# Performance work log

Hardware: AMD Instinct MI355X
Metric: run time of the kernel (lower is better)

## Reference

```python
import jax, jax.numpy as jnp
import numpy as np

B, S, E, H = 2, 2048, 1024, 16
DH = E // H


def setup_inputs() -> dict:
    key = jax.random.key(0)
    ks = jax.random.split(key, 9)
    s = 1.0 / np.sqrt(E)
    return {
        "queries": jax.random.normal(ks[0], (B, S, E), dtype=jnp.float32),
        "keys": jax.random.normal(ks[1], (B, S, E), dtype=jnp.float32),
        "values": jax.random.normal(ks[2], (B, S, E), dtype=jnp.float32),
        "mask": jax.random.randint(ks[3], (B, 1, 1, S), 0, 2, dtype=jnp.int32),
        "Wq": jax.random.normal(ks[4], (E, E), dtype=jnp.float32) * s,
        "Wk": jax.random.normal(ks[5], (E, E), dtype=jnp.float32) * s,
        "Wv": jax.random.normal(ks[6], (E, E), dtype=jnp.float32) * s,
        "Wo": jax.random.normal(ks[7], (E, E), dtype=jnp.float32) * s,
        "bo": jax.random.normal(ks[8], (E,), dtype=jnp.float32) * s,
    }


def reference(queries, keys, values, mask, Wq, Wk, Wv, Wo, bo):
    n, d_q, _ = queries.shape
    d_k = keys.shape[1]
    # Linear projections (torch Linear: x @ W.T), then split into heads
    q = (queries @ Wq.T).reshape(n, d_q, H, DH)
    k = (keys @ Wk.T).reshape(n, d_k, H, DH)
    v = (values @ Wv.T).reshape(n, d_k, H, DH)
    # [n, H, d_q, d_k] attention scores
    energy = jnp.einsum("nqhd,nkhd->nhqk", q, k)
    energy = jnp.where(mask == 0, jnp.float32(-1e20), energy)
    # NOTE: original scales by sqrt(key seq length), not head dim -- kept faithful
    attn = jax.nn.softmax(energy / jnp.sqrt(jnp.float32(d_k)), axis=3)
    out = jnp.einsum("nhql,nlhd->nqhd", attn, v).reshape(n, d_q, E)
    return out @ Wo.T + bo
```

## Files before the change

### kernel.cpp

```cpp
#include <hip/hip_runtime.h>
#include <hip/hip_bf16.h>

#define BB 2
#define SS 2048
#define EE 1024
#define HH 16
#define DHH 64

using bf16x8 = __attribute__((ext_vector_type(8))) __bf16;
using f32x4  = __attribute__((ext_vector_type(4))) float;

#if __has_builtin(__builtin_amdgcn_exp2f)
#define EXP2(x) __builtin_amdgcn_exp2f(x)
#else
#define EXP2(x) __exp2f(x)
#endif

static __device__ __forceinline__ unsigned short f2bf(float f) {
    unsigned int u = __float_as_uint(f);
    u += 0x7FFFu + ((u >> 16) & 1u);
    return (unsigned short)(u >> 16);
}

static __device__ __forceinline__ unsigned int pk2bf(float lo, float hi) {
    union { __hip_bfloat162 h2; unsigned int u; } c;
    c.h2 = __float22bfloat162_rn(float2{lo, hi});
    return c.u;
}

static __device__ __forceinline__ void async_load16(const void* g, void* l) {
    __builtin_amdgcn_global_load_lds(
        (const __attribute__((address_space(1))) unsigned int*)g,
        (__attribute__((address_space(3))) unsigned int*)l, 16, 0, 0);
}

__global__ void cvt_kernel(const float* __restrict__ W0, const float* __restrict__ W1,
                           const float* __restrict__ W2, const float* __restrict__ W3,
                           const float* __restrict__ X0, const float* __restrict__ X1,
                           const float* __restrict__ X2,
                           unsigned short* __restrict__ Wb,
                           unsigned short* __restrict__ D0, unsigned short* __restrict__ D1,
                           unsigned short* __restrict__ D2)
{
    const int z = blockIdx.y;
    const float* src;
    unsigned short* dst;
    if (z < 4) {
        if (blockIdx.x >= 512) return;
        src = (z == 0) ? W0 : (z == 1) ? W1 : (z == 2) ? W2 : W3;
        dst = Wb + (size_t)z * 1048576;
    } else {
        src = (z == 4) ? X0 : (z == 5) ? X1 : X2;
        dst = (z == 4) ? D0 : (z == 5) ? D1 : D2;
    }
    const size_t base = (size_t)blockIdx.x * 2048 + (size_t)threadIdx.x * 8;
    const float4 f0 = *(const float4*)(src + base);
    const float4 f1 = *(const float4*)(src + base + 4);
    uint4 p;
    p.x = pk2bf(f0.x, f0.y); p.y = pk2bf(f0.z, f0.w);
    p.z = pk2bf(f1.x, f1.y); p.w = pk2bf(f1.z, f1.w);
    *(uint4*)(dst + base) = p;
}

template<int MT, int NT, bool BF16OUT, bool VT_Z2>
__global__ __launch_bounds__(256, 3)
void gemm_xwt(const unsigned short* __restrict__ X0, const unsigned short* __restrict__ X1,
              const unsigned short* __restrict__ X2,
              const unsigned short* __restrict__ W0, const unsigned short* __restrict__ W1,
              const unsigned short* __restrict__ W2,
              void* __restrict__ Y0, void* __restrict__ Y1, void* __restrict__ Y2,
              const float* __restrict__ bias, int M, int N, int K,
              float s0, float s1, float s2)
{
    constexpr int BK = 32;
    constexpr int NI = MT / 32;
    constexpr int NJ = NT / 32;
    __shared__ __align__(16) unsigned short As[2][MT * BK];
    __shared__ __align__(16) unsigned short Bs[2][NT * BK];

    const int z = blockIdx.z;
    const unsigned short* __restrict__ X = (z == 0) ? X0 : ((z == 1) ? X1 : X2);
    const unsigned short* __restrict__ W = (z == 0) ? W0 : ((z == 1) ? W1 : W2);
    void* __restrict__ Y                 = (z == 0) ? Y0 : ((z == 1) ? Y1 : Y2);
    const float ysc                      = (z == 0) ? s0 : ((z == 1) ? s1 : s2);

    const int tid  = threadIdx.x;
    const int lane = tid & 63;
    const int wave = tid >> 6;
    const int wm   = (wave >> 1) * (MT / 2);
    const int wn   = (wave & 1) * (NT / 2);
    const int m0   = blockIdx.y * MT;
    const int n0   = blockIdx.x * NT;
    const int l16  = lane & 15;
    const int quad = lane >> 4;

    const int arow = lane >> 2;
    const int akc  = (lane & 3) * 8;

    f32x4 acc[NI][NJ];
    #pragma unroll
    for (int i = 0; i < NI; i++)
        #pragma unroll
        for (int j = 0; j < NJ; j++) acc[i][j] = f32x4{0.f, 0.f, 0.f, 0.f};

    auto stage = [&](int k0, int buf) {
        #pragma unroll
        for (int j = 0; j < NT / 64; j++) {
            const int rr = wave * (NT / 4) + j * 16;
            async_load16(W + (size_t)(n0 + rr + arow) * K + k0 + akc, Bs[buf] + rr * BK);
        }
        #pragma unroll
        for (int j = 0; j < MT / 64; j++) {
            const int rr = wave * (MT / 4) + j * 16;
            async_load16(X + (size_t)(m0 + rr + arow) * K + k0 + akc, As[buf] + rr * BK);
        }
    };

    stage(0, 0);
    const int niter = K / BK;
    for (int i = 0; i < niter; i++) {
        const int cur = i & 1;
        __syncthreads();
        if (i + 1 < niter) stage((i + 1) * BK, cur ^ 1);

        bf16x8 afrag[NI], bfrag[NJ];
        #pragma unroll
        for (int ii = 0; ii < NI; ii++)
            afrag[ii] = *(const bf16x8*)(As[cur] + (wm + ii * 16 + l16) * BK + quad * 8);
        #pragma unroll
        for (int j = 0; j < NJ; j++)
            bfrag[j] = *(const bf16x8*)(Bs[cur] + (wn + j * 16 + l16) * BK + quad * 8);
        #pragma unroll
        for (int ii = 0; ii < NI; ii++)
            #pragma unroll
            for (int j = 0; j < NJ; j++)
                acc[ii][j] = __builtin_amdgcn_mfma_f32_16x16x32_bf16(afrag[ii], bfrag[j], acc[ii][j], 0, 0, 0);
    }

    if (BF16OUT && VT_Z2 && z == 2) {
        #pragma unroll
        for (int i = 0; i < NI; i++) {
            const int row0 = m0 + wm + i * 16 + quad * 4;
            const int bb   = row0 >> 11;
            const int sx   = row0 & (SS - 1);
            #pragma unroll
            for (int j = 0; j < NJ; j++) {
                const int col = n0 + wn + j * 16 + l16;
                uint2 pck;
                pck.x = pk2bf(acc[i][j][0], acc[i][j][1]);
                pck.y = pk2bf(acc[i][j][2], acc[i][j][3]);
                *(uint2*)((unsigned short*)Y + (size_t)(bb * EE + col) * SS + sx) = pck;
            }
        }
    } else {
        #pragma unroll
        for (int i = 0; i < NI; i++) {
            #pragma unroll
            for (int j = 0; j < NJ; j++) {
                #pragma unroll
                for (int r = 0; r < 4; r++) {
                    const int row = m0 + wm + i * 16 + quad * 4 + r;
                    const int col = n0 + wn + j * 16 + l16;
                    const float v = acc[i][j][r];
                    if (BF16OUT) {
                        ((unsigned short*)Y)[(size_t)row * N + col] = f2bf(v * ysc);
                    } else {
                        ((float*)Y)[(size_t)row * N + col] = v + bias[col];
                    }
                }
            }
        }
    }
}

__global__ __launch_bounds__(256, 2)
void attn_kernel(const unsigned short* __restrict__ Qb,
                 const unsigned short* __restrict__ Kb,
                 const unsigned short* __restrict__ Vt,
                 const int* __restrict__ mask,
                 unsigned short* __restrict__ AO)
{
    constexpr int LDK = 68;
    constexpr int LDV = 68;
    constexpr int LDP = 68;
    __shared__ __align__(16) unsigned short Ks[64 * LDK];
    __shared__ __align__(16) unsigned short Vs[64 * LDV];
    __shared__ __align__(16) unsigned short Ps[4 * 32 * LDP];
    __shared__ __align__(16) float Msf[64];

    const int tid  = threadIdx.x;
    const int lane = tid & 63;
    const int wave = tid >> 6;
    const int l16  = lane & 15;
    const int quad = lane >> 4;

    const int bh = blockIdx.y;
    const int b  = bh >> 4;
    const int h  = bh & 15;
    const int q0 = blockIdx.x * 128 + wave * 32;

    bf16x8 qf[2][2];
    #pragma unroll
    for (int g = 0; g < 2; g++) {
        const unsigned short* qptr = Qb + (size_t)(b * SS + q0 + g * 16 + l16) * EE + h * DHH;
        qf[g][0] = *(const bf16x8*)(qptr + quad * 8);
        qf[g][1] = *(const bf16x8*)(qptr + 32 + quad * 8);
    }

    float lsum[2] = {0.f, 0.f};
    f32x4 o_acc[2][4];
    #pragma unroll
    for (int g = 0; g < 2; g++)
        #pragma unroll
        for (int j = 0; j < 4; j++) o_acc[g][j] = f32x4{0.f, 0.f, 0.f, 0.f};

    unsigned short* Pw = Ps + wave * 32 * LDP;

    const int srow = tid >> 2;
    const int sc   = (tid & 3) * 16;

    uint4 kr0, kr1, vr0, vr1;
    int   mr = 0;
    auto gload = [&](int t0) {
        const unsigned short* kg = Kb + (size_t)(b * SS + t0 + srow) * EE + h * DHH + sc;
        kr0 = *(const uint4*)(kg);
        kr1 = *(const uint4*)(kg + 8);
        const unsigned short* vg = Vt + (size_t)(b * EE + h * DHH + srow) * SS + t0 + sc;
        vr0 = *(const uint4*)(vg);
        vr1 = *(const uint4*)(vg + 8);
        if (tid < 64) mr = mask[b * SS + t0 + tid];
    };
    gload(0);

    for (int t0 = 0; t0 < SS; t0 += 64) {
        __syncthreads();
        *(uint4*)(Ks + srow * LDK + sc)     = kr0;
        *(uint4*)(Ks + srow * LDK + sc + 8) = kr1;
        *(uint4*)(Vs + srow * LDV + sc)     = vr0;
        *(uint4*)(Vs + srow * LDV + sc + 8) = vr1;
        if (tid < 64) Msf[tid] = mr ? 0.0f : -150.0f;
        __syncthreads();

        if (t0 + 64 < SS) gload(t0 + 64);

        #pragma unroll
        for (int nt = 0; nt < 4; nt++) {
            bf16x8 kf0 = *(const bf16x8*)(Ks + (nt * 16 + l16) * LDK + quad * 8);
            bf16x8 kf1 = *(const bf16x8*)(Ks + (nt * 16 + l16) * LDK + 32 + quad * 8);
            const f32x4 cinit = *(const f32x4*)(Msf + nt * 16 + quad * 4);
            #pragma unroll
            for (int g = 0; g < 2; g++) {
                f32x4 a = __builtin_amdgcn_mfma_f32_16x16x32_bf16(kf0, qf[g][0], cinit, 0, 0, 0);
                a = __builtin_amdgcn_mfma_f32_16x16x32_bf16(kf1, qf[g][1], a, 0, 0, 0);
                const float p0 = EXP2(a[0]);
                const float p1 = EXP2(a[1]);
                const float p2 = EXP2(a[2]);
                const float p3 = EXP2(a[3]);
                lsum[g] += (p0 + p1) + (p2 + p3);
                uint2 pck;
                pck.x = pk2bf(p0, p1);
                pck.y = pk2bf(p2, p3);
                *(uint2*)(Pw + (g * 16 + l16) * LDP + nt * 16 + quad * 4) = pck;
            }
        }

        __builtin_amdgcn_s_waitcnt(0xC07F);

        #pragma unroll
        for (int s2 = 0; s2 < 2; s2++) {
            bf16x8 pf0 = *(const bf16x8*)(Pw + l16 * LDP + s2 * 32 + quad * 8);
            bf16x8 pf1 = *(const bf16x8*)(Pw + (16 + l16) * LDP + s2 * 32 + quad * 8);
            #pragma unroll
            for (int jg = 0; jg < 4; jg++) {
                bf16x8 vf = *(const bf16x8*)(Vs + (jg * 16 + l16) * LDV + s2 * 32 + quad * 8);
                o_acc[0][jg] = __builtin_amdgcn_mfma_f32_16x16x32_bf16(vf, pf0, o_acc[0][jg], 0, 0, 0);
                o_acc[1][jg] = __builtin_amdgcn_mfma_f32_16x16x32_bf16(vf, pf1, o_acc[1][jg], 0, 0, 0);
            }
        }
    }

    #pragma unroll
    for (int g = 0; g < 2; g++) {
        float ls = lsum[g];
        ls += __shfl_xor(ls, 16, 64);
        ls += __shfl_xor(ls, 32, 64);
        const float rl = 1.0f / ls;
        const size_t orow = (size_t)(b * SS + q0 + g * 16 + l16) * EE + h * DHH;
        #pragma unroll
        for (int jg = 0; jg < 4; jg++) {
            uint2 pck;
            pck.x = pk2bf(o_acc[g][jg][0] * rl, o_acc[g][jg][1] * rl);
            pck.y = pk2bf(o_acc[g][jg][2] * rl, o_acc[g][jg][3] * rl);
            *(uint2*)(AO + orow + jg * 16 + quad * 4) = pck;
        }
    }
}

extern "C" void kernel_launch(void* const* d_in, const int* in_sizes, int n_in,
                              void* d_out, int out_size, void* d_ws, size_t ws_size,
                              hipStream_t stream)
{
    (void)in_sizes; (void)n_in; (void)out_size; (void)ws_size;
    const float* queries = (const float*)d_in[0];
    const float* keys    = (const float*)d_in[1];
    const float* values  = (const float*)d_in[2];
    const int*   mask    = (const int*)d_in[3];
    const float* Wq      = (const float*)d_in[4];
    const float* Wk      = (const float*)d_in[5];
    const float* Wv      = (const float*)d_in[6];
    const float* Wo      = (const float*)d_in[7];
    const float* bo      = (const float*)d_in[8];

    const size_t NE = (size_t)BB * SS * EE;
    const size_t WE = (size_t)EE * EE;

    unsigned short* Xq  = (unsigned short*)d_out;
    unsigned short* Xk  = Xq + NE;
    unsigned short* Wb  = (unsigned short*)d_ws;
    unsigned short* Xv  = Wb + 4 * WE;
    unsigned short* Qb  = Xv + NE;
    unsigned short* Kb  = Qb + NE;
    unsigned short* Vtb = Kb + NE;
    unsigned short* AOb = Xv;

    const int M = BB * SS, N = EE, K = EE;
    const float qscale = 0.022097086912079608f * 1.4426950408889634f;

    cvt_kernel<<<dim3(2048, 7), 256, 0, stream>>>(
        Wq, Wk, Wv, Wo, queries, keys, values, Wb, Xq, Xk, Xv);

    dim3 gproj(N / 128, M / 128, 3);
    gemm_xwt<128, 128, true, true><<<gproj, 256, 0, stream>>>(
        Xq, Xk, Xv, Wb, Wb + WE, Wb + 2 * WE,
        (void*)Qb, (void*)Kb, (void*)Vtb, nullptr, M, N, K,
        qscale, 1.0f, 1.0f);

    attn_kernel<<<dim3(SS / 128, BB * HH), 256, 0, stream>>>(Qb, Kb, Vtb, mask, AOb);

    dim3 gout(N / 64, M / 64, 1);
    gemm_xwt<64, 64, false, false><<<gout, 256, 0, stream>>>(
        AOb, AOb, AOb, Wb + 3 * WE, Wb + 3 * WE, Wb + 3 * WE,
        d_out, d_out, d_out, bo, M, N, K, 1.0f, 1.0f, 1.0f);
}
```

Baseline: 242.6 us.

## Double attention key tile to 128 and remap blocks for XCD-local head grouping

Raises the attention key/value tile from 64 to 128 keys per iteration, which halves the number of barrier pairs and loop iterations and issues more global loads per prefetch. It also flattens the grid to one dimension and remaps the block index so that consecutive blocks cover different (batch, head) pairs, apparently so blocks sharing K/V land together for cache locality. The cost is more LDS per block (larger K, V and P buffers) and more registers for the prefetch, which may reduce occupancy.

After: 267.4 us. 1.1x slower.

```diff
diff --git a/kernel.cpp b/kernel.cpp
--- a/kernel.cpp
+++ b/kernel.cpp
@@ -180,13 +180,14 @@
                  const int* __restrict__ mask,
                  unsigned short* __restrict__ AO)
 {
+    constexpr int TK  = 128;
     constexpr int LDK = 68;
-    constexpr int LDV = 68;
-    constexpr int LDP = 68;
-    __shared__ __align__(16) unsigned short Ks[64 * LDK];
+    constexpr int LDV = 136;
+    constexpr int LDP = 136;
+    __shared__ __align__(16) unsigned short Ks[TK * LDK];
     __shared__ __align__(16) unsigned short Vs[64 * LDV];
     __shared__ __align__(16) unsigned short Ps[4 * 32 * LDP];
-    __shared__ __align__(16) float Msf[64];
+    __shared__ __align__(16) float Msf[TK];
 
     const int tid  = threadIdx.x;
     const int lane = tid & 63;
@@ -194,10 +195,12 @@
     const int l16  = lane & 15;
     const int quad = lane >> 4;
 
-    const int bh = blockIdx.y;
+    const int linear = blockIdx.x;
+    const int bh     = (linear & 7) + 8 * ((linear >> 3) & 3);
+    const int qblk   = linear >> 5;
     const int b  = bh >> 4;
     const int h  = bh & 15;
-    const int q0 = blockIdx.x * 128 + wave * 32;
+    const int q0 = qblk * 128 + wave * 32;
 
     bf16x8 qf[2][2];
     #pragma unroll
@@ -216,35 +219,39 @@
 
     unsigned short* Pw = Ps + wave * 32 * LDP;
 
-    const int srow = tid >> 2;
-    const int sc   = (tid & 3) * 16;
-
-    uint4 kr0, kr1, vr0, vr1;
+    const int krow = tid >> 1;
+    const int kc   = (tid & 1) * 32;
+    const int vrow = tid >> 2;
+    const int vc   = (tid & 3) * 32;
+
+    uint4 kr[4], vr[4];
     int   mr = 0;
     auto gload = [&](int t0) {
-        const unsigned short* kg = Kb + (size_t)(b * SS + t0 + srow) * EE + h * DHH + sc;
-        kr0 = *(const uint4*)(kg);
-        kr1 = *(const uint4*)(kg + 8);
-        const unsigned short* vg = Vt + (size_t)(b * EE + h * DHH + srow) * SS + t0 + sc;
-        vr0 = *(const uint4*)(vg);
-        vr1 = *(const uint4*)(vg + 8);
-        if (tid < 64) mr = mask[b * SS + t0 + tid];
+        const unsigned short* kg = Kb + (size_t)(b * SS + t0 + krow) * EE + h * DHH + kc;
+        const unsigned short* vg = Vt + (size_t)(b * EE + h * DHH + vrow) * SS + t0 + vc;
+        #pragma unroll
+        for (int j = 0; j < 4; j++) {
+            kr[j] = *(const uint4*)(kg + j * 8);
+            vr[j] = *(const uint4*)(vg + j * 8);
+        }
+        if (tid < TK) mr = mask[b * SS + t0 + tid];
     };
     gload(0);
 
-    for (int t0 = 0; t0 < SS; t0 += 64) {
+    for (int t0 = 0; t0 < SS; t0 += TK) {
         __syncthreads();
-        *(uint4*)(Ks + srow * LDK + sc)     = kr0;
-        *(uint4*)(Ks + srow * LDK + sc + 8) = kr1;
-        *(uint4*)(Vs + srow * LDV + sc)     = vr0;
-        *(uint4*)(Vs + srow * LDV + sc + 8) = vr1;
-        if (tid < 64) Msf[tid] = mr ? 0.0f : -150.0f;
+        #pragma unroll
+        for (int j = 0; j < 4; j++) {
+            *(uint4*)(Ks + krow * LDK + kc + j * 8) = kr[j];
+            *(uint4*)(Vs + vrow * LDV + vc + j * 8) = vr[j];
+        }
+        if (tid < TK) Msf[tid] = mr ? 0.0f : -150.0f;
         __syncthreads();
 
-        if (t0 + 64 < SS) gload(t0 + 64);
-
-        #pragma unroll
-        for (int nt = 0; nt < 4; nt++) {
+        if (t0 + TK < SS) gload(t0 + TK);
+
+        #pragma unroll
+        for (int nt = 0; nt < 8; nt++) {
             bf16x8 kf0 = *(const bf16x8*)(Ks + (nt * 16 + l16) * LDK + quad * 8);
             bf16x8 kf1 = *(const bf16x8*)(Ks + (nt * 16 + l16) * LDK + 32 + quad * 8);
             const f32x4 cinit = *(const f32x4*)(Msf + nt * 16 + quad * 4);
@@ -267,7 +274,7 @@
         __builtin_amdgcn_s_waitcnt(0xC07F);
 
         #pragma unroll
-        for (int s2 = 0; s2 < 2; s2++) {
+        for (int s2 = 0; s2 < 4; s2++) {
             bf16x8 pf0 = *(const bf16x8*)(Pw + l16 * LDP + s2 * 32 + quad * 8);
             bf16x8 pf1 = *(const bf16x8*)(Pw + (16 + l16) * LDP + s2 * 32 + quad * 8);
             #pragma unroll
@@ -335,7 +342,7 @@
         (void*)Qb, (void*)Kb, (void*)Vtb, nullptr, M, N, K,
         qscale, 1.0f, 1.0f);
 
-    attn_kernel<<<dim3(SS / 128, BB * HH), 256, 0, stream>>>(Qb, Kb, Vtb, mask, AOb);
+    attn_kernel<<<dim3((SS / 128) * BB * HH), 256, 0, stream>>>(Qb, Kb, Vtb, mask, AOb);
 
     dim3 gout(N / 64, M / 64, 1);
     gemm_xwt<64, 64, false, false><<<gout, 256, 0, stream>>>(
```
